# Kernel tuning notes

Measured on AMD Instinct MI355X. Metric: run time of the kernel, lower is better.

The kernel has to match this reference:

```python
import jax, jax.numpy as jnp
import numpy as np

B, R, D, P = 32, 512, 256, 5532  # images, rois/image, feat dim, num_pids
NEG_INF = -1e30

def setup_inputs() -> dict:
    key = jax.random.key(0)
    k1, k2, k3 = jax.random.split(key, 3)
    inputs = jax.random.normal(k1, (B * R, D), dtype=jnp.float32)
    cls_scores = jax.random.uniform(k2, (B * R, 1), dtype=jnp.float32)
    roi_label = jax.random.randint(k3, (B, R), 0, P + 1)  # 0 = background -> label -1
    return {"inputs": inputs, "cls_scores": cls_scores, "roi_label": roi_label}

def reference(inputs, cls_scores, roi_label):
    x = (inputs * cls_scores).reshape(B, R, D)          # scale features by cls score
    label = roi_label - 1                               # [B,R], -1 = background
    valid = label >= 0                                  # keep labeled ROIs only
    lbl = jnp.where(valid, label, 0)

    # per-image per-pid mean prototypes via one segmented reduction
    seg = (jnp.arange(B)[:, None] * P + lbl).reshape(-1)             # [B*R]
    w = valid.reshape(-1).astype(x.dtype)
    sums = jax.ops.segment_sum(x.reshape(-1, D) * w[:, None], seg, num_segments=B * P)
    counts = jax.ops.segment_sum(w, seg, num_segments=B * P)          # [B*P]
    proto = sums / jnp.maximum(counts, 1.0)[:, None]
    proto = proto / jnp.maximum(jnp.linalg.norm(proto, axis=-1, keepdims=True), 1e-12)
    proto = jax.lax.stop_gradient(proto).reshape(B, P, D)            # .detach() in torch
    present = (counts > 0).reshape(B, P)                              # unique labels per image

    # project each ROI feature onto its image's prototypes
    logits = jnp.einsum('brd,bpd->brp', x, proto)                     # [B,R,P]
    logits = jnp.where(present[:, None, :], logits, NEG_INF)          # softmax over unique labels only
    logp = jax.nn.log_softmax(logits, axis=-1)
    nll = -jnp.take_along_axis(logp, lbl[..., None], axis=-1)[..., 0] # [B,R]
    nll = jnp.where(valid, nll, 0.0)
    n_valid = jnp.maximum(jnp.sum(valid).astype(x.dtype), 1.0)
    return jnp.sum(nll) / n_valid
```

## Files before the change

kernel.cpp:

```cpp
#include <hip/hip_runtime.h>
#include <math.h>

#define Bn 32
#define Rn 512
#define Dn 256
#define Pn 5532
#define MAXU 512

#define TRr 32
#define TCc 128
#define KCs 64
#define NSTG (Dn / KCs)
#define NBLK ((Rn / TRr) * Bn)

#define PBF_OFF    0
#define PBF_WORDS  (Bn*MAXU*Dn/2)
#define LBLC_OFF   (PBF_OFF + PBF_WORDS)
#define CCNT_OFF   (LBLC_OFF + Bn*Rn)
#define CURS_OFF   (CCNT_OFF + Bn*MAXU)
#define RLIST_OFF  (CURS_OFF + Bn*MAXU)
#define NUNIQ_OFF  (RLIST_OFF + Bn*Rn)
#define NVALID_OFF (NUNIQ_OFF + 32)
#define NLL_OFF    (NVALID_OFF + 32)
#define TICK_OFF   (NLL_OFF + 1)

typedef short short8 __attribute__((ext_vector_type(8)));
typedef short short4v __attribute__((ext_vector_type(4)));
typedef float floatx4 __attribute__((ext_vector_type(4)));

__device__ __forceinline__ unsigned short bf16r(float f) {
    union { float f; unsigned int u; } c; c.f = f;
    return (unsigned short)((c.u + 0x7FFFu + ((c.u >> 16) & 1u)) >> 16);
}
__device__ __forceinline__ float bfu2f(unsigned int hi16) {
    union { unsigned int u; float f; } c; c.u = hi16;
    return c.f;
}

__device__ __forceinline__ void async16(void* lds, const void* g) {
    auto* l3 = reinterpret_cast<__attribute__((address_space(3))) unsigned int*>(
                   reinterpret_cast<size_t>(lds));
    auto* g1 = reinterpret_cast<const __attribute__((address_space(1))) unsigned int*>(
                   reinterpret_cast<size_t>(g));
    __builtin_amdgcn_global_load_lds(g1, l3, 16, 0, 0);
}

__global__ __launch_bounds__(1024) void k1_compact(
    const int* __restrict__ roi_label,
    int* __restrict__ lblc_arr, int* __restrict__ ccnt, int* __restrict__ cursor,
    int* __restrict__ rlist, int* __restrict__ nuniq, int* __restrict__ nvalid_arr,
    int* __restrict__ zwords)
{
    __shared__ int cnt_lds[Pn];
    __shared__ int cmap_lds[Pn];
    __shared__ int curs_lds[MAXU];
    __shared__ int wpres[16], wcnt[16];

    const int b = blockIdx.x;
    const int t = threadIdx.x;
    const int lane = t & 63, wid = t >> 6;

    if (b == 0 && t == 0) { zwords[0] = 0; zwords[1] = 0; }

    for (int i = t; i < Pn; i += 1024) cnt_lds[i] = 0;
    __syncthreads();
    int mylbl = -1;
    if (t < Rn) {
        mylbl = roi_label[b * Rn + t] - 1;
        if (mylbl >= 0) atomicAdd(&cnt_lds[mylbl], 1);
    }
    __syncthreads();

    int basePres = 0, baseCnt = 0;
    for (int i0 = 0; i0 < Pn; i0 += 1024) {
        int i = i0 + t;
        int cnt = (i < Pn) ? cnt_lds[i] : 0;
        bool pres = cnt > 0;
        unsigned long long mask = __ballot(pres);
        int pfx_pres = __popcll(mask & ((1ULL << lane) - 1ULL));
        int v = cnt;
        #pragma unroll
        for (int off = 1; off < 64; off <<= 1) {
            int u = __shfl_up(v, off);
            if (lane >= off) v += u;
        }
        int pfx_cnt = v - cnt;
        if (lane == 63) { wpres[wid] = __popcll(mask); wcnt[wid] = v; }
        __syncthreads();
        int woffP = 0, totP = 0, woffC = 0, totC = 0;
        #pragma unroll
        for (int w = 0; w < 16; ++w) {
            int p = wpres[w], c = wcnt[w];
            if (w < wid) { woffP += p; woffC += c; }
            totP += p; totC += c;
        }
        if (pres) {
            int c = basePres + woffP + pfx_pres;
            cmap_lds[i] = c;
            ccnt[b * MAXU + c] = cnt;
            curs_lds[c] = baseCnt + woffC + pfx_cnt;
        }
        basePres += totP; baseCnt += totC;
        __syncthreads();
    }
    if (t < Rn) {
        int lc = (mylbl >= 0) ? cmap_lds[mylbl] : -1;
        lblc_arr[b * Rn + t] = lc;
        if (lc >= 0) {
            int pos = atomicAdd(&curs_lds[lc], 1);
            rlist[b * Rn + pos] = t;
        }
    }
    __syncthreads();
    if (t < MAXU && t < basePres)
        cursor[b * MAXU + t] = curs_lds[t];
    if (t == 0) { nuniq[b] = basePres; nvalid_arr[b] = baseCnt; }
}

__global__ __launch_bounds__(256) void k2_proto(
    const float* __restrict__ inputs, const float* __restrict__ cls,
    const int* __restrict__ nuniq, const int* __restrict__ ccnt,
    const int* __restrict__ cursor, const int* __restrict__ rlist,
    unsigned short* __restrict__ pbf)
{
    const int lane = threadIdx.x & 63, wv = threadIdx.x >> 6;
    const int h = blockIdx.x;
    const int xcd = h & 7, widx = h >> 3;
    const int b = xcd + 8 * (widx >> 7);
    const int inner = widx & 127;
    int c = inner * 4 + wv;
    int s = b * MAXU + c;
    if (c >= nuniq[b]) return;
    int cnt = ccnt[s];
    int start = cursor[s] - cnt;
    float a0 = 0.f, a1 = 0.f, a2 = 0.f, a3 = 0.f;
    for (int k = 0; k < cnt; ++k) {
        int row = b * Rn + rlist[b * Rn + start + k];
        float cw = cls[row];
        float4 v = *(const float4*)&inputs[(size_t)row * Dn + lane * 4];
        a0 += bfu2f(((unsigned)bf16r(v.x * cw)) << 16);
        a1 += bfu2f(((unsigned)bf16r(v.y * cw)) << 16);
        a2 += bfu2f(((unsigned)bf16r(v.z * cw)) << 16);
        a3 += bfu2f(((unsigned)bf16r(v.w * cw)) << 16);
    }
    float inv = 1.0f / (float)cnt;
    a0 *= inv; a1 *= inv; a2 *= inv; a3 *= inv;
    float ss = a0*a0 + a1*a1 + a2*a2 + a3*a3;
    #pragma unroll
    for (int off = 32; off > 0; off >>= 1) ss += __shfl_xor(ss, off);
    float sc = 1.0f / fmaxf(sqrtf(ss), 1e-12f);
    short4v o;
    o[0] = (short)bf16r(a0 * sc); o[1] = (short)bf16r(a1 * sc);
    o[2] = (short)bf16r(a2 * sc); o[3] = (short)bf16r(a3 * sc);
    *(short4v*)&pbf[(size_t)s * Dn + lane * 4] = o;
}

__global__ __launch_bounds__(256, 2) void k3_loss(
    const float* __restrict__ inputs, const float* __restrict__ cls,
    const unsigned short* __restrict__ pbf,
    const int* __restrict__ lblc_arr, const int* __restrict__ nuniq,
    const int* __restrict__ nvalid_arr,
    float* __restrict__ nll, int* __restrict__ tick, float* __restrict__ out)
{
    __shared__ __align__(16) unsigned short xs[TRr * Dn];
    __shared__ __align__(16) unsigned short psb[2][TCc * KCs];
    __shared__ int lblc[TRr];
    __shared__ float es_l[4][TRr];
    __shared__ float ds_l[4][TRr];

    const int t = threadIdx.x;
    const int lane = t & 63, w = t >> 6;
    const int q = lane >> 4, r15 = lane & 15;
    const int h = blockIdx.x;
    const int xcd = h & 7, widx = h >> 3;
    const int b  = xcd + 8 * (widx >> 4);
    const int rt = widx & 15;
    const int roiBase = rt * TRr;
    const int U = nuniq[b];
    const int nch = (U <= 0) ? 1 : ((U + TCc - 1) >> 7);

    if (t < TRr) lblc[t] = lblc_arr[b * Rn + roiBase + t];

#define ISSUE_PS(PC, ST, BUF)                                                \
    do {                                                                     \
        _Pragma("unroll")                                                    \
        for (int i_ = 0; i_ < 4; ++i_) {                                     \
            int ci_ = i_ * 256 + w * 64 + lane;                              \
            int pr_ = ci_ >> 3, gp_ = ci_ & 7;                               \
            int g_ = gp_ ^ (pr_ & 7);                                        \
            async16(&psb[BUF][(i_ * 256 + w * 64) * 8],                      \
                    pbf + (size_t)(b * MAXU + (PC) * TCc + pr_) * Dn         \
                        + (ST) * KCs + g_ * 8);                              \
        }                                                                    \
    } while (0)

    ISSUE_PS(0, 0, 0);

    {
        const int row = t >> 3, seg = t & 7;
        const size_t gbase = (size_t)(b * Rn + roiBase + row) * Dn + seg * 32;
        const float cw = cls[b * Rn + roiBase + row];
        #pragma unroll
        for (int jj = 0; jj < 4; ++jj) {
            float4 v0 = *(const float4*)&inputs[gbase + jj * 8];
            float4 v1 = *(const float4*)&inputs[gbase + jj * 8 + 4];
            short8 o;
            o[0] = (short)bf16r(v0.x * cw); o[1] = (short)bf16r(v0.y * cw);
            o[2] = (short)bf16r(v0.z * cw); o[3] = (short)bf16r(v0.w * cw);
            o[4] = (short)bf16r(v1.x * cw); o[5] = (short)bf16r(v1.y * cw);
            o[6] = (short)bf16r(v1.z * cw); o[7] = (short)bf16r(v1.w * cw);
            int gpos = (seg * 4 + jj) ^ (row & 7);
            *(short8*)&xs[row * Dn + gpos * 8] = o;
        }
    }
    __syncthreads();

    short8 areg[2][8];
    #pragma unroll
    for (int mt = 0; mt < 2; ++mt)
        #pragma unroll
        for (int kcs = 0; kcs < 8; ++kcs) {
            int row = mt * 16 + r15;
            int gpos = (kcs * 4 + q) ^ (row & 7);
            areg[mt][kcs] = *(const short8*)&xs[row * Dn + gpos * 8];
        }

    int lcr[2][4];
    float esum[2][4], dsum[2][4];
    #pragma unroll
    for (int mt = 0; mt < 2; ++mt)
        #pragma unroll
        for (int reg = 0; reg < 4; ++reg) {
            lcr[mt][reg] = lblc[mt * 16 + q * 4 + reg];
            esum[mt][reg] = 0.f; dsum[mt][reg] = 0.f;
        }

    for (int pc = 0; pc < nch; ++pc) {
        floatx4 acc[2][2];
        #pragma unroll
        for (int mt = 0; mt < 2; ++mt) {
            acc[mt][0] = (floatx4)0.f; acc[mt][1] = (floatx4)0.f;
        }

        #pragma unroll
        for (int st = 0; st < NSTG; ++st) {
            const int cur = st & 1;
            __syncthreads();
            int ns = pc * NSTG + st + 1;
            if (ns < nch * NSTG) ISSUE_PS(ns >> 2, ns & 3, cur ^ 1);
            #pragma unroll
            for (int kk = 0; kk < 2; ++kk) {
                short8 bb[2];
                #pragma unroll
                for (int nt = 0; nt < 2; ++nt) {
                    int r = w * 32 + nt * 16 + r15;
                    int gpos = (kk * 4 + q) ^ (r & 7);
                    bb[nt] = *(const short8*)&psb[cur][r * KCs + gpos * 8];
                }
                #pragma unroll
                for (int mt = 0; mt < 2; ++mt) {
                    acc[mt][0] = __builtin_amdgcn_mfma_f32_16x16x32_bf16(
                        areg[mt][st * 2 + kk], bb[0], acc[mt][0], 0, 0, 0);
                    acc[mt][1] = __builtin_amdgcn_mfma_f32_16x16x32_bf16(
                        areg[mt][st * 2 + kk], bb[1], acc[mt][1], 0, 0, 0);
                }
            }
        }

        #pragma unroll
        for (int nt = 0; nt < 2; ++nt) {
            int c = pc * TCc + w * 32 + nt * 16 + r15;
            bool v = c < U;
            #pragma unroll
            for (int mt = 0; mt < 2; ++mt)
                #pragma unroll
                for (int reg = 0; reg < 4; ++reg) {
                    float d = acc[mt][nt][reg];
                    if (v) esum[mt][reg] += __expf(d);
                    if (c == lcr[mt][reg]) dsum[mt][reg] += d;
                }
        }
    }
#undef ISSUE_PS

    #pragma unroll
    for (int mt = 0; mt < 2; ++mt)
        #pragma unroll
        for (int reg = 0; reg < 4; ++reg) {
            float e = esum[mt][reg], d = dsum[mt][reg];
            #pragma unroll
            for (int off = 1; off < 16; off <<= 1) {
                e += __shfl_xor(e, off);
                d += __shfl_xor(d, off);
            }
            if (r15 == 0) {
                int row = mt * 16 + q * 4 + reg;
                es_l[w][row] = e;
                ds_l[w][row] = d;
            }
        }
    __syncthreads();
    if (t < TRr) {
        float es = es_l[0][t] + es_l[1][t] + es_l[2][t] + es_l[3][t];
        float ds = ds_l[0][t] + ds_l[1][t] + ds_l[2][t] + ds_l[3][t];
        float val = (lblc[t] >= 0) ? (__logf(es) - ds) : 0.f;
        #pragma unroll
        for (int off = 1; off < 32; off <<= 1) val += __shfl_xor(val, off);
        if (t == 0) {
            atomicAdd(nll, val);
            __threadfence();
            int old = atomicAdd(tick, 1);
            if (old == NBLK - 1) {
                float total = atomicAdd(nll, 0.0f);
                int nv = 0;
                #pragma unroll
                for (int i = 0; i < Bn / 4; ++i) {
                    int4 vv = ((const int4*)nvalid_arr)[i];
                    nv += vv.x + vv.y + vv.z + vv.w;
                }
                out[0] = total / fmaxf((float)nv, 1.0f);
            }
        }
    }
}

extern "C" void kernel_launch(void* const* d_in, const int* in_sizes, int n_in,
                              void* d_out, int out_size, void* d_ws, size_t ws_size,
                              hipStream_t stream) {
    const float* inputs = (const float*)d_in[0];
    const float* cls    = (const float*)d_in[1];
    const int*   roi    = (const int*)d_in[2];
    int* wsi   = (int*)d_ws;
    float* out = (float*)d_out;

    unsigned short* pbf = (unsigned short*)(wsi + PBF_OFF);
    int*   lblc   = wsi + LBLC_OFF;
    int*   ccnt   = wsi + CCNT_OFF;
    int*   cursor = wsi + CURS_OFF;
    int*   rlist  = wsi + RLIST_OFF;
    int*   nuniq  = wsi + NUNIQ_OFF;
    int*   nvalid = wsi + NVALID_OFF;
    float* nll    = (float*)(wsi + NLL_OFF);
    int*   tick   = wsi + TICK_OFF;

    k1_compact<<<Bn, 1024, 0, stream>>>(roi, lblc, ccnt, cursor, rlist,
                                        nuniq, nvalid, wsi + NLL_OFF);
    k2_proto<<<(Bn * MAXU) / 4, 256, 0, stream>>>(inputs, cls, nuniq, ccnt,
                                                  cursor, rlist, pbf);
    k3_loss<<<NBLK, 256, 0, stream>>>(inputs, cls, pbf, lblc, nuniq, nvalid,
                                      nll, tick, out);
}
```

Measured before the change: 104.7 us.

## Load prototypes directly to registers and simplify label compaction with atomics

The loss kernel drops the LDS double-buffered async staging of prototype tiles. Each wave now loads its B fragments for a whole 128-column chunk straight from global memory into registers, which removes the per-stage block barriers. The compaction kernel replaces the ordered prefix scan over all pid labels with atomic first-seen slot assignment plus a short scan over at most 512 slots. The trade-off is more global traffic per wave and higher register pressure, with no overlap of loads and MFMA across chunks, and slot ordering is now nondeterministic.

```diff
diff --git a/kernel.cpp b/kernel.cpp
--- a/kernel.cpp
+++ b/kernel.cpp
@@ -10,7 +10,6 @@
 #define TRr 32
 #define TCc 128
 #define KCs 64
-#define NSTG (Dn / KCs)
 #define NBLK ((Rn / TRr) * Bn)
 
 #define PBF_OFF    0
@@ -37,24 +36,18 @@
     return c.f;
 }
 
-__device__ __forceinline__ void async16(void* lds, const void* g) {
-    auto* l3 = reinterpret_cast<__attribute__((address_space(3))) unsigned int*>(
-                   reinterpret_cast<size_t>(lds));
-    auto* g1 = reinterpret_cast<const __attribute__((address_space(1))) unsigned int*>(
-                   reinterpret_cast<size_t>(g));
-    __builtin_amdgcn_global_load_lds(g1, l3, 16, 0, 0);
-}
-
 __global__ __launch_bounds__(1024) void k1_compact(
     const int* __restrict__ roi_label,
     int* __restrict__ lblc_arr, int* __restrict__ ccnt, int* __restrict__ cursor,
     int* __restrict__ rlist, int* __restrict__ nuniq, int* __restrict__ nvalid_arr,
     int* __restrict__ zwords)
 {
-    __shared__ int cnt_lds[Pn];
-    __shared__ int cmap_lds[Pn];
-    __shared__ int curs_lds[MAXU];
-    __shared__ int wpres[16], wcnt[16];
+    __shared__ int cnt_l[Pn];
+    __shared__ int slot_l[Pn];
+    __shared__ int scnt[MAXU];
+    __shared__ int scur[MAXU];
+    __shared__ int wtot[16];
+    __shared__ int uctr;
 
     const int b = blockIdx.x;
     const int t = threadIdx.x;
@@ -62,59 +55,58 @@
 
     if (b == 0 && t == 0) { zwords[0] = 0; zwords[1] = 0; }
 
-    for (int i = t; i < Pn; i += 1024) cnt_lds[i] = 0;
-    __syncthreads();
-    int mylbl = -1;
+    for (int i = t; i < Pn; i += 1024) cnt_l[i] = 0;
+    if (t < MAXU) scnt[t] = 0;
+    if (t == 0) uctr = 0;
+    __syncthreads();
+
+    int l = -1;
     if (t < Rn) {
-        mylbl = roi_label[b * Rn + t] - 1;
-        if (mylbl >= 0) atomicAdd(&cnt_lds[mylbl], 1);
-    }
-    __syncthreads();
-
-    int basePres = 0, baseCnt = 0;
-    for (int i0 = 0; i0 < Pn; i0 += 1024) {
-        int i = i0 + t;
-        int cnt = (i < Pn) ? cnt_lds[i] : 0;
-        bool pres = cnt > 0;
-        unsigned long long mask = __ballot(pres);
-        int pfx_pres = __popcll(mask & ((1ULL << lane) - 1ULL));
-        int v = cnt;
-        #pragma unroll
-        for (int off = 1; off < 64; off <<= 1) {
-            int u = __shfl_up(v, off);
-            if (lane >= off) v += u;
-        }
-        int pfx_cnt = v - cnt;
-        if (lane == 63) { wpres[wid] = __popcll(mask); wcnt[wid] = v; }
-        __syncthreads();
-        int woffP = 0, totP = 0, woffC = 0, totC = 0;
-        #pragma unroll
-        for (int w = 0; w < 16; ++w) {
-            int p = wpres[w], c = wcnt[w];
-            if (w < wid) { woffP += p; woffC += c; }
-            totP += p; totC += c;
-        }
-        if (pres) {
-            int c = basePres + woffP + pfx_pres;
-            cmap_lds[i] = c;
-            ccnt[b * MAXU + c] = cnt;
-            curs_lds[c] = baseCnt + woffC + pfx_cnt;
-        }
-        basePres += totP; baseCnt += totC;
-        __syncthreads();
-    }
+        l = roi_label[b * Rn + t] - 1;
+        if (l >= 0) {
+            if (atomicAdd(&cnt_l[l], 1) == 0)
+                slot_l[l] = atomicAdd(&uctr, 1);
+        }
+    }
+    __syncthreads();
+    int lc = -1;
     if (t < Rn) {
-        int lc = (mylbl >= 0) ? cmap_lds[mylbl] : -1;
+        lc = (l >= 0) ? slot_l[l] : -1;
         lblc_arr[b * Rn + t] = lc;
-        if (lc >= 0) {
-            int pos = atomicAdd(&curs_lds[lc], 1);
-            rlist[b * Rn + pos] = t;
-        }
-    }
-    __syncthreads();
-    if (t < MAXU && t < basePres)
-        cursor[b * MAXU + t] = curs_lds[t];
-    if (t == 0) { nuniq[b] = basePres; nvalid_arr[b] = baseCnt; }
+        if (lc >= 0) atomicAdd(&scnt[lc], 1);
+    }
+    __syncthreads();
+    const int U = uctr;
+
+    int v = (t < MAXU) ? scnt[t] : 0;
+    int vs = v;
+    #pragma unroll
+    for (int off = 1; off < 64; off <<= 1) {
+        int u = __shfl_up(vs, off);
+        if (lane >= off) vs += u;
+    }
+    if (lane == 63) wtot[wid] = vs;
+    __syncthreads();
+    int woff = 0, tot = 0;
+    #pragma unroll
+    for (int w = 0; w < 16; ++w) {
+        int c = wtot[w];
+        if (w < wid) woff += c;
+        tot += c;
+    }
+    if (t < MAXU) scur[t] = woff + vs - v;
+    __syncthreads();
+
+    if (t < Rn && lc >= 0) {
+        int pos = atomicAdd(&scur[lc], 1);
+        rlist[b * Rn + pos] = t;
+    }
+    __syncthreads();
+    if (t < MAXU && t < U) {
+        ccnt[b * MAXU + t]   = scnt[t];
+        cursor[b * MAXU + t] = scur[t];
+    }
+    if (t == 0) { nuniq[b] = U; nvalid_arr[b] = tot; }
 }
 
 __global__ __launch_bounds__(256) void k2_proto(
@@ -163,7 +155,6 @@
     float* __restrict__ nll, int* __restrict__ tick, float* __restrict__ out)
 {
     __shared__ __align__(16) unsigned short xs[TRr * Dn];
-    __shared__ __align__(16) unsigned short psb[2][TCc * KCs];
     __shared__ int lblc[TRr];
     __shared__ float es_l[4][TRr];
     __shared__ float ds_l[4][TRr];
@@ -181,21 +172,6 @@
 
     if (t < TRr) lblc[t] = lblc_arr[b * Rn + roiBase + t];
 
-#define ISSUE_PS(PC, ST, BUF)                                                \
-    do {                                                                     \
-        _Pragma("unroll")                                                    \
-        for (int i_ = 0; i_ < 4; ++i_) {                                     \
-            int ci_ = i_ * 256 + w * 64 + lane;                              \
-            int pr_ = ci_ >> 3, gp_ = ci_ & 7;                               \
-            int g_ = gp_ ^ (pr_ & 7);                                        \
-            async16(&psb[BUF][(i_ * 256 + w * 64) * 8],                      \
-                    pbf + (size_t)(b * MAXU + (PC) * TCc + pr_) * Dn         \
-                        + (ST) * KCs + g_ * 8);                              \
-        }                                                                    \
-    } while (0)
-
-    ISSUE_PS(0, 0, 0);
-
     {
         const int row = t >> 3, seg = t & 7;
         const size_t gbase = (size_t)(b * Rn + roiBase + row) * Dn + seg * 32;
@@ -235,35 +211,35 @@
             esum[mt][reg] = 0.f; dsum[mt][reg] = 0.f;
         }
 
+    const unsigned short* pw0 =
+        pbf + (size_t)(b * MAXU + w * 32 + r15) * Dn + q * 8;
+
     for (int pc = 0; pc < nch; ++pc) {
+        const unsigned short* p0 = pw0 + (size_t)pc * TCc * Dn;
+        const unsigned short* p1 = p0 + 16 * Dn;
+        short8 b0[8], b1[8];
+        #pragma unroll
+        for (int st = 0; st < 4; ++st)
+            #pragma unroll
+            for (int kk = 0; kk < 2; ++kk) {
+                int off = st * KCs + kk * 32;
+                b0[st * 2 + kk] = *(const short8*)&p0[off];
+                b1[st * 2 + kk] = *(const short8*)&p1[off];
+            }
+
         floatx4 acc[2][2];
         #pragma unroll
         for (int mt = 0; mt < 2; ++mt) {
             acc[mt][0] = (floatx4)0.f; acc[mt][1] = (floatx4)0.f;
         }
-
-        #pragma unroll
-        for (int st = 0; st < NSTG; ++st) {
-            const int cur = st & 1;
-            __syncthreads();
-            int ns = pc * NSTG + st + 1;
-            if (ns < nch * NSTG) ISSUE_PS(ns >> 2, ns & 3, cur ^ 1);
+        #pragma unroll
+        for (int f = 0; f < 8; ++f) {
             #pragma unroll
-            for (int kk = 0; kk < 2; ++kk) {
-                short8 bb[2];
-                #pragma unroll
-                for (int nt = 0; nt < 2; ++nt) {
-                    int r = w * 32 + nt * 16 + r15;
-                    int gpos = (kk * 4 + q) ^ (r & 7);
-                    bb[nt] = *(const short8*)&psb[cur][r * KCs + gpos * 8];
-                }
-                #pragma unroll
-                for (int mt = 0; mt < 2; ++mt) {
-                    acc[mt][0] = __builtin_amdgcn_mfma_f32_16x16x32_bf16(
-                        areg[mt][st * 2 + kk], bb[0], acc[mt][0], 0, 0, 0);
-                    acc[mt][1] = __builtin_amdgcn_mfma_f32_16x16x32_bf16(
-                        areg[mt][st * 2 + kk], bb[1], acc[mt][1], 0, 0, 0);
-                }
+            for (int mt = 0; mt < 2; ++mt) {
+                acc[mt][0] = __builtin_amdgcn_mfma_f32_16x16x32_bf16(
+                    areg[mt][f], b0[f], acc[mt][0], 0, 0, 0);
+                acc[mt][1] = __builtin_amdgcn_mfma_f32_16x16x32_bf16(
+                    areg[mt][f], b1[f], acc[mt][1], 0, 0, 0);
             }
         }
 
@@ -281,7 +257,6 @@
                 }
         }
     }
-#undef ISSUE_PS
 
     #pragma unroll
     for (int mt = 0; mt < 2; ++mt)
```

New measurement: 106.1 us. No clear change (+1.3%).
